# Kernel optimization log

Measured on AMD Instinct MI355X. Metric: run time of the kernel, lower is better.

Reference implementation:

```python
import jax, jax.numpy as jnp
import numpy as np

B, N, D_MODEL, H = 4, 2048, 1024, 16  # batch, seq, model dim, heads


def setup_inputs() -> dict:
    key = jax.random.key(0)
    k1, k2, k3 = jax.random.split(key, 3)
    x = jax.random.normal(k1, (B, N, D_MODEL), dtype=jnp.float32)
    # nn.Linear weights: [out_features, in_features]; scaled for stability
    Wqkv = jax.random.normal(k2, (3 * D_MODEL, D_MODEL), dtype=jnp.float32) * 0.02
    bqkv = jnp.zeros((3 * D_MODEL,), dtype=jnp.float32)
    Wo = jax.random.normal(k3, (D_MODEL, D_MODEL), dtype=jnp.float32) * 0.02
    bo = jnp.zeros((D_MODEL,), dtype=jnp.float32)
    return {"x": x, "Wqkv": Wqkv, "bqkv": bqkv, "Wo": Wo, "bo": bo}


def reference(x, Wqkv, bqkv, Wo, bo):
    b, n, _ = x.shape
    qkv = x @ Wqkv.T + bqkv                      # [b, n, 3*d_model]
    # rearrange 'b n (h d) -> b h n d' with h heads, then chunk into q,k,v
    qkv = qkv.reshape(b, n, H, -1).transpose(0, 2, 1, 3)  # [b, h, n, 3*dh]
    q, k, v = jnp.split(qkv, 3, axis=-1)          # each [b, h, n, dh]
    scale = k.shape[-1] ** 0.5
    scores = jnp.einsum('bhqd,bhkd->bhqk', q, k) / scale
    attn = jax.nn.softmax(scores, axis=-1)
    out = jnp.einsum('bhqk,bhkd->bhqd', attn, v)  # [b, h, n, dh]
    out = out.transpose(0, 2, 1, 3).reshape(b, n, -1)  # 'b h n d -> b n (h d)'
    return out @ Wo.T + bo
```

## Files before the change

### kernel.cpp

```cpp
#include <hip/hip_runtime.h>
#include <hip/hip_bf16.h>

using bf16 = __hip_bfloat16;
typedef __attribute__((ext_vector_type(8))) __bf16 bf16x8;
typedef __attribute__((ext_vector_type(4))) float f32x4;
typedef __attribute__((ext_vector_type(16))) float f32x16;
typedef __attribute__((ext_vector_type(4))) unsigned u32x4;

#define MFMA16(a, b, c) __builtin_amdgcn_mfma_f32_16x16x32_bf16((a), (b), (c), 0, 0, 0)
#define MFMA32(a, b, c) __builtin_amdgcn_mfma_f32_32x32x16_bf16((a), (b), (c), 0, 0, 0)

#define WAITV4 asm volatile("s_waitcnt vmcnt(4)" ::: "memory")
#define WAITV0 asm volatile("s_waitcnt vmcnt(0)" ::: "memory")
#define WAITL0 asm volatile("s_waitcnt lgkmcnt(0)" ::: "memory")
#define BAR    __builtin_amdgcn_s_barrier()
#define SCHED0 __builtin_amdgcn_sched_barrier(0)

static __device__ __forceinline__ void gload_lds16(const bf16* g, bf16* l) {
    __builtin_amdgcn_global_load_lds(
        (__attribute__((address_space(1))) void*)(bf16*)(g),
        (__attribute__((address_space(3))) void*)(l), 16, 0, 0);
}

static __device__ __forceinline__ unsigned cvtpk(float lo, float hi) {
    unsigned r;
    asm("v_cvt_pk_bf16_f32 %0, %1, %2" : "=v"(r) : "v"(lo), "v"(hi));
    return r;
}

__global__ void cvt_all(const float* __restrict__ x, const float* __restrict__ wq,
                        const float* __restrict__ wo,
                        bf16* __restrict__ xb, bf16* __restrict__ wqb, bf16* __restrict__ wob) {
    int b = blockIdx.x;
    const float* src;
    bf16* dst;
    long i;
    if (b < 8192)       { src = x;  dst = xb;  i = (long)b * 256 + threadIdx.x; }
    else if (b < 11264) { src = wq; dst = wqb; i = (long)(b - 8192) * 256 + threadIdx.x; }
    else                { src = wo; dst = wob; i = (long)(b - 11264) * 256 + threadIdx.x; }
    float4 v = ((const float4*)src)[i];
    bf16 t[4];
    t[0] = __float2bfloat16(v.x);
    t[1] = __float2bfloat16(v.y);
    t[2] = __float2bfloat16(v.z);
    t[3] = __float2bfloat16(v.w);
    *(uint2*)(dst + 4l * i) = *(uint2*)t;
}

#define GEMM_STAGE(AB, BB, K0)                                             \
    do {                                                                   \
        gload_lds16(Ab + (long)srow * K + (K0) + scol, (AB) + t * 8);      \
        gload_lds16(Ab + (long)(srow + 64) * K + (K0) + scol, (AB) + 2048 + t * 8); \
        gload_lds16(Bb + (long)srow * K + (K0) + scol, (BB) + t * 8);      \
        gload_lds16(Bb + (long)(srow + 64) * K + (K0) + scol, (BB) + 2048 + t * 8); \
    } while (0)

#define GEMM_COMPUTE(AB, BB)                                               \
    do {                                                                   \
        bf16x8 af[4], bfv[4];                                              \
        _Pragma("unroll") for (int mi4 = 0; mi4 < 4; mi4++)                \
            af[mi4] = *(const bf16x8*)((AB) + (wm * 64 + mi4 * 16 + r) * 32 + q * 8); \
        _Pragma("unroll") for (int ni4 = 0; ni4 < 4; ni4++)                \
            bfv[ni4] = *(const bf16x8*)((BB) + (wn * 64 + ni4 * 16 + r) * 32 + q * 8); \
        __builtin_amdgcn_s_setprio(1);                                     \
        _Pragma("unroll") for (int mi4 = 0; mi4 < 4; mi4++)                \
            _Pragma("unroll") for (int ni4 = 0; ni4 < 4; ni4++)            \
                acc[mi4][ni4] = MFMA16(af[mi4], bfv[ni4], acc[mi4][ni4]);  \
        __builtin_amdgcn_s_setprio(0);                                     \
    } while (0)

#define GEMM_MAIN_LOOP                                                     \
    GEMM_STAGE(A0, B0, 0);                                                 \
    GEMM_STAGE(A1, B1, 32);                                                \
    for (int k0 = 0; k0 < K - 64; k0 += 64) {                              \
        WAITV4; BAR; SCHED0;                                               \
        GEMM_COMPUTE(A0, B0);                                              \
        WAITL0; BAR; SCHED0;                                               \
        GEMM_STAGE(A0, B0, k0 + 64);                                       \
        WAITV4; BAR; SCHED0;                                               \
        GEMM_COMPUTE(A1, B1);                                              \
        WAITL0; BAR; SCHED0;                                               \
        if (k0 + 96 < K) GEMM_STAGE(A1, B1, k0 + 96);                      \
    }                                                                      \
    WAITV4; BAR; SCHED0;                                                   \
    GEMM_COMPUTE(A0, B0);                                                  \
    WAITV0; BAR; SCHED0;                                                   \
    GEMM_COMPUTE(A1, B1);

__global__ void gemm_qkv(const bf16* __restrict__ A, const bf16* __restrict__ B,
                         const float* __restrict__ bias,
                         bf16* __restrict__ Qo, bf16* __restrict__ Ko, bf16* __restrict__ Vt) {
    const int K = 1024;
    __shared__ bf16 smem[16384];
    bf16* A0 = smem;
    bf16* B0 = smem + 4096;
    bf16* A1 = smem + 8192;
    bf16* B1 = smem + 12288;
    int t = threadIdx.x;
    int lane = t & 63;
    int wave = t >> 6;
    int wm = wave >> 1, wn = wave & 1;
    int r = lane & 15, q = lane >> 4;
    int lin = blockIdx.x;
    int xcd = lin & 7, rr_ = lin >> 3;
    int mi = xcd * 8 + (rr_ & 7);
    int ni = rr_ >> 3;
    long m0 = (long)mi * 128;
    long n0 = (long)ni * 128;
    const bf16* Ab = A + m0 * K;
    const bf16* Bb = B + n0 * K;

    f32x4 acc[4][4] = {};

    int srow = t >> 2;
    int scol = (t & 3) << 3;

    GEMM_MAIN_LOOP

#pragma unroll
    for (int ni4 = 0; ni4 < 4; ni4++) {
        int n = (int)n0 + wn * 64 + ni4 * 16 + r;
        float bn = bias[n];
        int h = n / 192;
        int rem = n % 192;
        int part = rem >> 6;
        int d = rem & 63;
#pragma unroll
        for (int mi4 = 0; mi4 < 4; mi4++) {
#pragma unroll
            for (int rr = 0; rr < 4; rr++) {
                int m = (int)m0 + wm * 64 + mi4 * 16 + q * 4 + rr;
                int b = m >> 11;
                int row = m & 2047;
                long bh = b * 16 + h;
                bf16 bv = __float2bfloat16(acc[mi4][ni4][rr] + bn);
                if (part == 0)      Qo[(bh * 2048 + row) * 64 + d] = bv;
                else if (part == 1) Ko[(bh * 2048 + row) * 64 + d] = bv;
                else                Vt[(bh * 64 + d) * 2048 + row] = bv;
            }
        }
    }
}


#define PACK8(S, OFF, OUTV) { \
    unsigned A0_ = cvtpk(S[OFF+0], S[OFF+1]); \
    unsigned B0_ = cvtpk(S[OFF+4], S[OFF+5]); \
    unsigned A1_ = cvtpk(S[OFF+2], S[OFF+3]); \
    unsigned B1_ = cvtpk(S[OFF+6], S[OFF+7]); \
    asm("v_permlane32_swap_b32 %0, %1" : "+v"(A0_), "+v"(B0_)); \
    asm("v_permlane32_swap_b32 %0, %1" : "+v"(A1_), "+v"(B1_)); \
    u32x4 W; W.x = A0_; W.y = A1_; W.z = B0_; W.w = B1_; \
    OUTV = __builtin_bit_cast(bf16x8, W); }

#define COMPUTE(KB, VB) do { \
    f32x16 sA = {}, sB = {}; \
    __builtin_amdgcn_s_setprio(1); \
    { \
        bf16x8 kA, kB; \
        kA = *(const bf16x8*)(KB + (0 * 64 + lane) * 8); \
        kB = *(const bf16x8*)(KB + (256 + 0 * 64 + lane) * 8); \
        sA = MFMA32(kA, qf0, sA);  sB = MFMA32(kB, qf0, sB); \
        kA = *(const bf16x8*)(KB + (1 * 64 + lane) * 8); \
        kB = *(const bf16x8*)(KB + (256 + 1 * 64 + lane) * 8); \
        sA = MFMA32(kA, qf1, sA);  sB = MFMA32(kB, qf1, sB); \
        kA = *(const bf16x8*)(KB + (2 * 64 + lane) * 8); \
        kB = *(const bf16x8*)(KB + (256 + 2 * 64 + lane) * 8); \
        sA = MFMA32(kA, qf2, sA);  sB = MFMA32(kB, qf2, sB); \
        kA = *(const bf16x8*)(KB + (3 * 64 + lane) * 8); \
        kB = *(const bf16x8*)(KB + (256 + 3 * 64 + lane) * 8); \
        sA = MFMA32(kA, qf3, sA);  sB = MFMA32(kB, qf3, sB); \
    } \
    __builtin_amdgcn_s_setprio(0); \
    float x0 = fmaxf(fmaxf(sA[0], sA[1]), fmaxf(sA[2], sA[3])); \
    float x1 = fmaxf(fmaxf(sA[4], sA[5]), fmaxf(sA[6], sA[7])); \
    float x2 = fmaxf(fmaxf(sA[8], sA[9]), fmaxf(sA[10], sA[11])); \
    float x3 = fmaxf(fmaxf(sA[12], sA[13]), fmaxf(sA[14], sA[15])); \
    float y0 = fmaxf(fmaxf(sB[0], sB[1]), fmaxf(sB[2], sB[3])); \
    float y1 = fmaxf(fmaxf(sB[4], sB[5]), fmaxf(sB[6], sB[7])); \
    float y2 = fmaxf(fmaxf(sB[8], sB[9]), fmaxf(sB[10], sB[11])); \
    float y3 = fmaxf(fmaxf(sB[12], sB[13]), fmaxf(sB[14], sB[15])); \
    float pm = fmaxf(fmaxf(fmaxf(x0, x1), fmaxf(x2, x3)), \
                     fmaxf(fmaxf(y0, y1), fmaxf(y2, y3))); \
    pm = fmaxf(pm, __shfl_xor(pm, 32)); \
    bool resc = !__all(pm <= mv + 8.0f); \
    if (resc) { \
        float mn = fmaxf(mv, pm); \
        float al = __builtin_amdgcn_exp2f((mv - mn) * C1); \
        mv = mn; \
        lv *= al; \
        _Pragma("unroll") for (int e = 0; e < 16; ++e) { o0[e] *= al; o1[e] *= al; } \
    } \
    float mc = mv * C1; \
    float ts = 0.f; \
    _Pragma("unroll") for (int e = 0; e < 16; ++e) { float p = __builtin_amdgcn_exp2f(sA[e] * C1 - mc); sA[e] = p; ts += p; } \
    _Pragma("unroll") for (int e = 0; e < 16; ++e) { float p = __builtin_amdgcn_exp2f(sB[e] * C1 - mc); sB[e] = p; ts += p; } \
    ts += __shfl_xor(ts, 32); \
    lv += ts; \
    bf16x8 pf0, pf1, pf2, pf3; \
    PACK8(sA, 0, pf0); PACK8(sA, 8, pf1); PACK8(sB, 0, pf2); PACK8(sB, 8, pf3); \
    __builtin_amdgcn_s_setprio(1); \
    { \
        bf16x8 vA, vB; \
        vA = *(const bf16x8*)(VB + (0 * 64 + lane) * 8); \
        vB = *(const bf16x8*)(VB + (256 + 0 * 64 + lane) * 8); \
        o0 = MFMA32(vA, pf0, o0);  o1 = MFMA32(vB, pf0, o1); \
        vA = *(const bf16x8*)(VB + (1 * 64 + lane) * 8); \
        vB = *(const bf16x8*)(VB + (256 + 1 * 64 + lane) * 8); \
        o0 = MFMA32(vA, pf1, o0);  o1 = MFMA32(vB, pf1, o1); \
        vA = *(const bf16x8*)(VB + (2 * 64 + lane) * 8); \
        vB = *(const bf16x8*)(VB + (256 + 2 * 64 + lane) * 8); \
        o0 = MFMA32(vA, pf2, o0);  o1 = MFMA32(vB, pf2, o1); \
        vA = *(const bf16x8*)(VB + (3 * 64 + lane) * 8); \
        vB = *(const bf16x8*)(VB + (256 + 3 * 64 + lane) * 8); \
        o0 = MFMA32(vA, pf3, o0);  o1 = MFMA32(vB, pf3, o1); \
    } \
    __builtin_amdgcn_s_setprio(0); \
} while (0)

__global__ __launch_bounds__(512, 4) void attn_fwd(const bf16* __restrict__ Q,
                                                   const bf16* __restrict__ Kg,
                                                   const bf16* __restrict__ Vt,
                                                   bf16* __restrict__ AO) {
    __shared__ bf16 smem[16384];
    bf16* K0 = smem;
    bf16* V0 = smem + 4096;
    bf16* K1 = smem + 8192;
    bf16* V1 = smem + 12288;
    const int t = threadIdx.x;
    const int lane = t & 63, wave = t >> 6;
    const int l31 = lane & 31, hi = lane >> 5;
    const int bid = blockIdx.x;
    const int xcd = bid & 7, idx = bid >> 3;
    const int bh = xcd * 8 + (idx >> 3);
    const int qt = idx & 7;
    const float C1 = 0.18033688011112042f;

    bf16x8 qf0, qf1, qf2, qf3;
    {
        const bf16* Qb = Q + ((long)bh * 2048 + qt * 256 + wave * 32 + l31) * 64 + hi * 8;
        qf0 = *(const bf16x8*)(Qb + 0);
        qf1 = *(const bf16x8*)(Qb + 16);
        qf2 = *(const bf16x8*)(Qb + 32);
        qf3 = *(const bf16x8*)(Qb + 48);
    }

    const bf16* Kh = Kg + (long)bh * 2048 * 64;
    const bf16* Vh = Vt + (long)bh * 64 * 2048;

    const int sr = ((t >> 8) << 5) + (t & 31);
    const int sc = ((t >> 6) & 3) * 16 + ((t >> 5) & 1) * 8;

    f32x16 o0 = {}, o1 = {};
    float mv = -1e30f, lv = 0.f;

    auto issue_stage = [&](bf16* Kb, bf16* Vb, int kv0) {
        gload_lds16(Kh + (long)(kv0 + sr) * 64 + sc, Kb + t * 8);
        gload_lds16(Vh + (long)sr * 2048 + kv0 + sc, Vb + t * 8);
    };

    issue_stage(K0, V0, 0);
    __syncthreads();

    for (int kv0 = 0;; kv0 += 128) {
        issue_stage(K1, V1, kv0 + 64);
        COMPUTE(K0, V0);
        __syncthreads();
        if (kv0 + 128 < 2048) issue_stage(K0, V0, kv0 + 128);
        COMPUTE(K1, V1);
        if (kv0 + 128 >= 2048) break;
        __syncthreads();
    }

    long bb = bh >> 4, hh = bh & 15;
    __syncthreads();
    float il = 1.f / lv;
    char* wbase = (char*)smem + wave * 4096 + l31 * 128;
#pragma unroll
    for (int j = 0; j < 4; ++j) {
        unsigned wlo = cvtpk(o0[4 * j] * il, o0[4 * j + 1] * il);
        unsigned whi = cvtpk(o0[4 * j + 2] * il, o0[4 * j + 3] * il);
        int b8 = 2 * j + hi;
        int b8s = b8 ^ ((l31 & 7) << 1);
        uint2 val; val.x = wlo; val.y = whi;
        *(uint2*)(wbase + b8s * 8) = val;
    }
#pragma unroll
    for (int j = 0; j < 4; ++j) {
        unsigned wlo = cvtpk(o1[4 * j] * il, o1[4 * j + 1] * il);
        unsigned whi = cvtpk(o1[4 * j + 2] * il, o1[4 * j + 3] * il);
        int b8 = 8 + 2 * j + hi;
        int b8s = b8 ^ ((l31 & 7) << 1);
        uint2 val; val.x = wlo; val.y = whi;
        *(uint2*)(wbase + b8s * 8) = val;
    }
    __syncthreads();
    {
        int rid = t >> 1, hf = t & 1;
        int wv = rid >> 5, qq = rid & 31;
        long orow = (long)qt * 256 + wv * 32 + qq;
        const char* rbase = (const char*)smem + wv * 4096 + qq * 128;
        bf16* dst = AO + (bb * 2048 + orow) * 1024 + hh * 64 + hf * 32;
#pragma unroll
        for (int k = 0; k < 4; ++k) {
            int b8 = hf * 8 + 2 * k;
            int b8s = b8 ^ ((qq & 7) << 1);
            int4 v = *(const int4*)(rbase + b8s * 8);
            *(int4*)(dst + k * 8) = v;
        }
    }
}

__global__ void gemm_out(const bf16* __restrict__ A, const bf16* __restrict__ B,
                         const float* __restrict__ bias, float* __restrict__ C) {
    const int K = 1024, N = 1024;
    __shared__ bf16 smem[16384];
    bf16* A0 = smem;
    bf16* B0 = smem + 4096;
    bf16* A1 = smem + 8192;
    bf16* B1 = smem + 12288;
    int t = threadIdx.x;
    int lane = t & 63;
    int wave = t >> 6;
    int wm = wave >> 1, wn = wave & 1;
    int r = lane & 15, q = lane >> 4;
    int lin = blockIdx.x;
    int xcd = lin & 7, rr_ = lin >> 3;
    int mi = xcd * 8 + (rr_ & 7);
    int ni = rr_ >> 3;
    long m0 = (long)mi * 128;
    long n0 = (long)ni * 128;
    const bf16* Ab = A + m0 * K;
    const bf16* Bb = B + n0 * K;

    f32x4 acc[4][4] = {};

    int srow = t >> 2;
    int scol = (t & 3) << 3;

    GEMM_MAIN_LOOP

#pragma unroll
    for (int ni4 = 0; ni4 < 4; ni4++) {
        int n = (int)n0 + wn * 64 + ni4 * 16 + r;
        float bn = bias[n];
#pragma unroll
        for (int mi4 = 0; mi4 < 4; mi4++) {
#pragma unroll
            for (int rr = 0; rr < 4; rr++) {
                long m = m0 + wm * 64 + mi4 * 16 + q * 4 + rr;
                C[m * N + n] = acc[mi4][ni4][rr] + bn;
            }
        }
    }
}

extern "C" void kernel_launch(void* const* d_in, const int* in_sizes, int n_in,
                              void* d_out, int out_size, void* d_ws, size_t ws_size,
                              hipStream_t stream) {
    const float* x    = (const float*)d_in[0];
    const float* Wqkv = (const float*)d_in[1];
    const float* bqkv = (const float*)d_in[2];
    const float* Wo   = (const float*)d_in[3];
    const float* bo   = (const float*)d_in[4];
    float* out = (float*)d_out;

    char* ws = (char*)d_ws;
    bf16* Xb  = (bf16*)(ws + 0);
    bf16* Wqb = (bf16*)(ws + 16777216);
    bf16* Wob = (bf16*)(ws + 23068672);
    bf16* Qb  = (bf16*)(ws + 25165824);
    bf16* Kb  = (bf16*)(ws + 41943040);
    bf16* Vtb = (bf16*)(ws + 58720256);
    bf16* AOb = (bf16*)(ws + 75497472);

    cvt_all<<<12288, 256, 0, stream>>>(x, Wqkv, Wo, Xb, Wqb, Wob);

    gemm_qkv<<<1536, 256, 0, stream>>>(Xb, Wqb, bqkv, Qb, Kb, Vtb);
    attn_fwd<<<512, 512, 0, stream>>>(Qb, Kb, Vtb, AOb);
    gemm_out<<<512, 256, 0, stream>>>(AOb, Wob, bo, out);
}
```

Before: 193.1 us.

## Process two 32-row query tiles per wave to reuse K/V loads

Each wave now handles 64 query rows, kept as two independent 32-row tiles with separate softmax state, so each K/V LDS fragment read feeds twice as many MFMAs. The grid shrinks from 512 to 256 blocks of 512 threads and launch bounds drop to 2 blocks per CU to make room for the doubled accumulators and Q fragments. The aim is to halve global and LDS traffic for K/V per query row and to interleave two independent MFMA chains. The costs are higher register pressure, lower occupancy, and only 256 blocks, which may underfill the GPU's 256 CUs and cause tail imbalance.

Result: no change. 196.7 us (+1.9%).

```diff
diff --git a/kernel.cpp b/kernel.cpp
--- a/kernel.cpp
+++ b/kernel.cpp
@@ -153,72 +153,112 @@
     u32x4 W; W.x = A0_; W.y = A1_; W.z = B0_; W.w = B1_; \
     OUTV = __builtin_bit_cast(bf16x8, W); }
 
-#define COMPUTE(KB, VB) do { \
-    f32x16 sA = {}, sB = {}; \
+#define SMAXP(SA, SB, O0, O1, MV, LV, PF0, PF1, PF2, PF3) do { \
+    float x0 = fmaxf(fmaxf(SA[0], SA[1]), fmaxf(SA[2], SA[3])); \
+    float x1 = fmaxf(fmaxf(SA[4], SA[5]), fmaxf(SA[6], SA[7])); \
+    float x2 = fmaxf(fmaxf(SA[8], SA[9]), fmaxf(SA[10], SA[11])); \
+    float x3 = fmaxf(fmaxf(SA[12], SA[13]), fmaxf(SA[14], SA[15])); \
+    float y0 = fmaxf(fmaxf(SB[0], SB[1]), fmaxf(SB[2], SB[3])); \
+    float y1 = fmaxf(fmaxf(SB[4], SB[5]), fmaxf(SB[6], SB[7])); \
+    float y2 = fmaxf(fmaxf(SB[8], SB[9]), fmaxf(SB[10], SB[11])); \
+    float y3 = fmaxf(fmaxf(SB[12], SB[13]), fmaxf(SB[14], SB[15])); \
+    float pm = fmaxf(fmaxf(fmaxf(x0, x1), fmaxf(x2, x3)), \
+                     fmaxf(fmaxf(y0, y1), fmaxf(y2, y3))); \
+    pm = fmaxf(pm, __shfl_xor(pm, 32)); \
+    bool resc = !__all(pm <= MV + 8.0f); \
+    if (resc) { \
+        float mn = fmaxf(MV, pm); \
+        float al = __builtin_amdgcn_exp2f((MV - mn) * C1); \
+        MV = mn; \
+        LV *= al; \
+        _Pragma("unroll") for (int e = 0; e < 16; ++e) { O0[e] *= al; O1[e] *= al; } \
+    } \
+    float mc = MV * C1; \
+    float ts = 0.f; \
+    _Pragma("unroll") for (int e = 0; e < 16; ++e) { float p = __builtin_amdgcn_exp2f(SA[e] * C1 - mc); SA[e] = p; ts += p; } \
+    _Pragma("unroll") for (int e = 0; e < 16; ++e) { float p = __builtin_amdgcn_exp2f(SB[e] * C1 - mc); SB[e] = p; ts += p; } \
+    ts += __shfl_xor(ts, 32); \
+    LV += ts; \
+    PACK8(SA, 0, PF0); PACK8(SA, 8, PF1); PACK8(SB, 0, PF2); PACK8(SB, 8, PF3); \
+} while (0)
+
+#define COMPUTE2(KB, VB) do { \
+    f32x16 sA0 = {}, sB0 = {}, sA1 = {}, sB1 = {}; \
     __builtin_amdgcn_s_setprio(1); \
     { \
         bf16x8 kA, kB; \
         kA = *(const bf16x8*)(KB + (0 * 64 + lane) * 8); \
         kB = *(const bf16x8*)(KB + (256 + 0 * 64 + lane) * 8); \
-        sA = MFMA32(kA, qf0, sA);  sB = MFMA32(kB, qf0, sB); \
+        sA0 = MFMA32(kA, qfA0, sA0);  sB0 = MFMA32(kB, qfA0, sB0); \
+        sA1 = MFMA32(kA, qfB0, sA1);  sB1 = MFMA32(kB, qfB0, sB1); \
         kA = *(const bf16x8*)(KB + (1 * 64 + lane) * 8); \
         kB = *(const bf16x8*)(KB + (256 + 1 * 64 + lane) * 8); \
-        sA = MFMA32(kA, qf1, sA);  sB = MFMA32(kB, qf1, sB); \
+        sA0 = MFMA32(kA, qfA1, sA0);  sB0 = MFMA32(kB, qfA1, sB0); \
+        sA1 = MFMA32(kA, qfB1, sA1);  sB1 = MFMA32(kB, qfB1, sB1); \
         kA = *(const bf16x8*)(KB + (2 * 64 + lane) * 8); \
         kB = *(const bf16x8*)(KB + (256 + 2 * 64 + lane) * 8); \
-        sA = MFMA32(kA, qf2, sA);  sB = MFMA32(kB, qf2, sB); \
+        sA0 = MFMA32(kA, qfA2, sA0);  sB0 = MFMA32(kB, qfA2, sB0); \
+        sA1 = MFMA32(kA, qfB2, sA1);  sB1 = MFMA32(kB, qfB2, sB1); \
         kA = *(const bf16x8*)(KB + (3 * 64 + lane) * 8); \
         kB = *(const bf16x8*)(KB + (256 + 3 * 64 + lane) * 8); \
-        sA = MFMA32(kA, qf3, sA);  sB = MFMA32(kB, qf3, sB); \
+        sA0 = MFMA32(kA, qfA3, sA0);  sB0 = MFMA32(kB, qfA3, sB0); \
+        sA1 = MFMA32(kA, qfB3, sA1);  sB1 = MFMA32(kB, qfB3, sB1); \
     } \
     __builtin_amdgcn_s_setprio(0); \
-    float x0 = fmaxf(fmaxf(sA[0], sA[1]), fmaxf(sA[2], sA[3])); \
-    float x1 = fmaxf(fmaxf(sA[4], sA[5]), fmaxf(sA[6], sA[7])); \
-    float x2 = fmaxf(fmaxf(sA[8], sA[9]), fmaxf(sA[10], sA[11])); \
-    float x3 = fmaxf(fmaxf(sA[12], sA[13]), fmaxf(sA[14], sA[15])); \
-    float y0 = fmaxf(fmaxf(sB[0], sB[1]), fmaxf(sB[2], sB[3])); \
-    float y1 = fmaxf(fmaxf(sB[4], sB[5]), fmaxf(sB[6], sB[7])); \
-    float y2 = fmaxf(fmaxf(sB[8], sB[9]), fmaxf(sB[10], sB[11])); \
-    float y3 = fmaxf(fmaxf(sB[12], sB[13]), fmaxf(sB[14], sB[15])); \
-    float pm = fmaxf(fmaxf(fmaxf(x0, x1), fmaxf(x2, x3)), \
-                     fmaxf(fmaxf(y0, y1), fmaxf(y2, y3))); \
-    pm = fmaxf(pm, __shfl_xor(pm, 32)); \
-    bool resc = !__all(pm <= mv + 8.0f); \
-    if (resc) { \
-        float mn = fmaxf(mv, pm); \
-        float al = __builtin_amdgcn_exp2f((mv - mn) * C1); \
-        mv = mn; \
-        lv *= al; \
-        _Pragma("unroll") for (int e = 0; e < 16; ++e) { o0[e] *= al; o1[e] *= al; } \
-    } \
-    float mc = mv * C1; \
-    float ts = 0.f; \
-    _Pragma("unroll") for (int e = 0; e < 16; ++e) { float p = __builtin_amdgcn_exp2f(sA[e] * C1 - mc); sA[e] = p; ts += p; } \
-    _Pragma("unroll") for (int e = 0; e < 16; ++e) { float p = __builtin_amdgcn_exp2f(sB[e] * C1 - mc); sB[e] = p; ts += p; } \
-    ts += __shfl_xor(ts, 32); \
-    lv += ts; \
-    bf16x8 pf0, pf1, pf2, pf3; \
-    PACK8(sA, 0, pf0); PACK8(sA, 8, pf1); PACK8(sB, 0, pf2); PACK8(sB, 8, pf3); \
+    bf16x8 p00, p01, p02, p03, p10, p11, p12, p13; \
+    SMAXP(sA0, sB0, o00, o01, mv0, lv0, p00, p01, p02, p03); \
+    SMAXP(sA1, sB1, o10, o11, mv1, lv1, p10, p11, p12, p13); \
     __builtin_amdgcn_s_setprio(1); \
     { \
         bf16x8 vA, vB; \
         vA = *(const bf16x8*)(VB + (0 * 64 + lane) * 8); \
         vB = *(const bf16x8*)(VB + (256 + 0 * 64 + lane) * 8); \
-        o0 = MFMA32(vA, pf0, o0);  o1 = MFMA32(vB, pf0, o1); \
+        o00 = MFMA32(vA, p00, o00);  o01 = MFMA32(vB, p00, o01); \
+        o10 = MFMA32(vA, p10, o10);  o11 = MFMA32(vB, p10, o11); \
         vA = *(const bf16x8*)(VB + (1 * 64 + lane) * 8); \
         vB = *(const bf16x8*)(VB + (256 + 1 * 64 + lane) * 8); \
-        o0 = MFMA32(vA, pf1, o0);  o1 = MFMA32(vB, pf1, o1); \
+        o00 = MFMA32(vA, p01, o00);  o01 = MFMA32(vB, p01, o01); \
+        o10 = MFMA32(vA, p11, o10);  o11 = MFMA32(vB, p11, o11); \
         vA = *(const bf16x8*)(VB + (2 * 64 + lane) * 8); \
         vB = *(const bf16x8*)(VB + (256 + 2 * 64 + lane) * 8); \
-        o0 = MFMA32(vA, pf2, o0);  o1 = MFMA32(vB, pf2, o1); \
+        o00 = MFMA32(vA, p02, o00);  o01 = MFMA32(vB, p02, o01); \
+        o10 = MFMA32(vA, p12, o10);  o11 = MFMA32(vB, p12, o11); \
         vA = *(const bf16x8*)(VB + (3 * 64 + lane) * 8); \
         vB = *(const bf16x8*)(VB + (256 + 3 * 64 + lane) * 8); \
-        o0 = MFMA32(vA, pf3, o0);  o1 = MFMA32(vB, pf3, o1); \
+        o00 = MFMA32(vA, p03, o00);  o01 = MFMA32(vB, p03, o01); \
+        o10 = MFMA32(vA, p13, o10);  o11 = MFMA32(vB, p13, o11); \
     } \
     __builtin_amdgcn_s_setprio(0); \
 } while (0)
 
-__global__ __launch_bounds__(512, 4) void attn_fwd(const bf16* __restrict__ Q,
+#define EPI(O0v, O1v, LVv, QBOFF) { \
+    __syncthreads(); \
+    float il = 1.f / LVv; \
+    char* wbase = (char*)smem + wave * 4096 + l31 * 128; \
+    _Pragma("unroll") for (int j = 0; j < 4; ++j) { \
+        unsigned wlo = cvtpk(O0v[4 * j] * il, O0v[4 * j + 1] * il); \
+        unsigned whi = cvtpk(O0v[4 * j + 2] * il, O0v[4 * j + 3] * il); \
+        int b8 = 2 * j + hi; int b8s = b8 ^ ((l31 & 7) << 1); \
+        uint2 val; val.x = wlo; val.y = whi; \
+        *(uint2*)(wbase + b8s * 8) = val; } \
+    _Pragma("unroll") for (int j = 0; j < 4; ++j) { \
+        unsigned wlo = cvtpk(O1v[4 * j] * il, O1v[4 * j + 1] * il); \
+        unsigned whi = cvtpk(O1v[4 * j + 2] * il, O1v[4 * j + 3] * il); \
+        int b8 = 8 + 2 * j + hi; int b8s = b8 ^ ((l31 & 7) << 1); \
+        uint2 val; val.x = wlo; val.y = whi; \
+        *(uint2*)(wbase + b8s * 8) = val; } \
+    __syncthreads(); \
+    { int rid = t >> 1, hf = t & 1; \
+      int wv = rid >> 5, qq = rid & 31; \
+      long orow = (long)qt * 512 + wv * 64 + (QBOFF) + qq; \
+      const char* rbase = (const char*)smem + wv * 4096 + qq * 128; \
+      bf16* dst = AO + (bb * 2048 + orow) * 1024 + hh * 64 + hf * 32; \
+      _Pragma("unroll") for (int k = 0; k < 4; ++k) { \
+          int b8 = hf * 8 + 2 * k; int b8s = b8 ^ ((qq & 7) << 1); \
+          int4 v = *(const int4*)(rbase + b8s * 8); \
+          *(int4*)(dst + k * 8) = v; } } }
+
+__global__ __launch_bounds__(512, 2) void attn_fwd(const bf16* __restrict__ Q,
                                                    const bf16* __restrict__ Kg,
                                                    const bf16* __restrict__ Vt,
                                                    bf16* __restrict__ AO) {
@@ -232,17 +272,22 @@
     const int l31 = lane & 31, hi = lane >> 5;
     const int bid = blockIdx.x;
     const int xcd = bid & 7, idx = bid >> 3;
-    const int bh = xcd * 8 + (idx >> 3);
-    const int qt = idx & 7;
+    const int bh = xcd * 8 + (idx >> 2);
+    const int qt = idx & 3;
     const float C1 = 0.18033688011112042f;
 
-    bf16x8 qf0, qf1, qf2, qf3;
+    bf16x8 qfA0, qfA1, qfA2, qfA3, qfB0, qfB1, qfB2, qfB3;
     {
-        const bf16* Qb = Q + ((long)bh * 2048 + qt * 256 + wave * 32 + l31) * 64 + hi * 8;
-        qf0 = *(const bf16x8*)(Qb + 0);
-        qf1 = *(const bf16x8*)(Qb + 16);
-        qf2 = *(const bf16x8*)(Qb + 32);
-        qf3 = *(const bf16x8*)(Qb + 48);
+        const bf16* Qb = Q + ((long)bh * 2048 + qt * 512 + wave * 64 + l31) * 64 + hi * 8;
+        qfA0 = *(const bf16x8*)(Qb + 0);
+        qfA1 = *(const bf16x8*)(Qb + 16);
+        qfA2 = *(const bf16x8*)(Qb + 32);
+        qfA3 = *(const bf16x8*)(Qb + 48);
+        const bf16* Qb2 = Qb + 32 * 64;
+        qfB0 = *(const bf16x8*)(Qb2 + 0);
+        qfB1 = *(const bf16x8*)(Qb2 + 16);
+        qfB2 = *(const bf16x8*)(Qb2 + 32);
+        qfB3 = *(const bf16x8*)(Qb2 + 48);
     }
 
     const bf16* Kh = Kg + (long)bh * 2048 * 64;
@@ -251,8 +296,8 @@
     const int sr = ((t >> 8) << 5) + (t & 31);
     const int sc = ((t >> 6) & 3) * 16 + ((t >> 5) & 1) * 8;
 
-    f32x16 o0 = {}, o1 = {};
-    float mv = -1e30f, lv = 0.f;
+    f32x16 o00 = {}, o01 = {}, o10 = {}, o11 = {};
+    float mv0 = -1e30f, mv1 = -1e30f, lv0 = 0.f, lv1 = 0.f;
 
     auto issue_stage = [&](bf16* Kb, bf16* Vb, int kv0) {
         gload_lds16(Kh + (long)(kv0 + sr) * 64 + sc, Kb + t * 8);
@@ -264,51 +309,17 @@
 
     for (int kv0 = 0;; kv0 += 128) {
         issue_stage(K1, V1, kv0 + 64);
-        COMPUTE(K0, V0);
+        COMPUTE2(K0, V0);
         __syncthreads();
         if (kv0 + 128 < 2048) issue_stage(K0, V0, kv0 + 128);
-        COMPUTE(K1, V1);
+        COMPUTE2(K1, V1);
         if (kv0 + 128 >= 2048) break;
         __syncthreads();
     }
 
     long bb = bh >> 4, hh = bh & 15;
-    __syncthreads();
-    float il = 1.f / lv;
-    char* wbase = (char*)smem + wave * 4096 + l31 * 128;
-#pragma unroll
-    for (int j = 0; j < 4; ++j) {
-        unsigned wlo = cvtpk(o0[4 * j] * il, o0[4 * j + 1] * il);
-        unsigned whi = cvtpk(o0[4 * j + 2] * il, o0[4 * j + 3] * il);
-        int b8 = 2 * j + hi;
-        int b8s = b8 ^ ((l31 & 7) << 1);
-        uint2 val; val.x = wlo; val.y = whi;
-        *(uint2*)(wbase + b8s * 8) = val;
-    }
-#pragma unroll
-    for (int j = 0; j < 4; ++j) {
-        unsigned wlo = cvtpk(o1[4 * j] * il, o1[4 * j + 1] * il);
-        unsigned whi = cvtpk(o1[4 * j + 2] * il, o1[4 * j + 3] * il);
-        int b8 = 8 + 2 * j + hi;
-        int b8s = b8 ^ ((l31 & 7) << 1);
-        uint2 val; val.x = wlo; val.y = whi;
-        *(uint2*)(wbase + b8s * 8) = val;
-    }
-    __syncthreads();
-    {
-        int rid = t >> 1, hf = t & 1;
-        int wv = rid >> 5, qq = rid & 31;
-        long orow = (long)qt * 256 + wv * 32 + qq;
-        const char* rbase = (const char*)smem + wv * 4096 + qq * 128;
-        bf16* dst = AO + (bb * 2048 + orow) * 1024 + hh * 64 + hf * 32;
-#pragma unroll
-        for (int k = 0; k < 4; ++k) {
-            int b8 = hf * 8 + 2 * k;
-            int b8s = b8 ^ ((qq & 7) << 1);
-            int4 v = *(const int4*)(rbase + b8s * 8);
-            *(int4*)(dst + k * 8) = v;
-        }
-    }
+    EPI(o00, o01, lv0, 0);
+    EPI(o10, o11, lv1, 32);
 }
 
 __global__ void gemm_out(const bf16* __restrict__ A, const bf16* __restrict__ B,
@@ -377,6 +388,6 @@
     cvt_all<<<12288, 256, 0, stream>>>(x, Wqkv, Wo, Xb, Wqb, Wob);
 
     gemm_qkv<<<1536, 256, 0, stream>>>(Xb, Wqb, bqkv, Qb, Kb, Vtb);
-    attn_fwd<<<512, 512, 0, stream>>>(Qb, Kb, Vtb, AOb);
+    attn_fwd<<<256, 512, 0, stream>>>(Qb, Kb, Vtb, AOb);
     gemm_out<<<512, 256, 0, stream>>>(AOb, Wob, bo, out);
 }
```
